# Optimization experiments

Measured on AMD Instinct MI355X. Metric: run time of the kernel, lower is better.

## Reference

```python
import jax, jax.numpy as jnp
import numpy as np

B, T, K = 128, 2048, 96  # batch, seq_len, num_tags


def setup_inputs() -> dict:
    key = jax.random.key(0)
    k1, k2, k3 = jax.random.split(key, 3)
    inputs = jax.random.normal(k1, (B, T, K), dtype=jnp.float32)
    tags = jax.random.randint(k2, (B, T), 0, K, dtype=jnp.int32)
    mask = jnp.ones((B, T), dtype=jnp.int32)
    transitions = jax.random.normal(k3, (K, K), dtype=jnp.float32) * 0.1
    return {"inputs": inputs, "tags": tags, "mask": mask, "transitions": transitions}


def _input_likelihood(inputs, mask, transitions):
    # Forward algorithm (log partition), no start/end transitions.
    logits_t = jnp.swapaxes(inputs, 0, 1)                     # [T,B,K]
    mask_t = jnp.swapaxes(mask, 0, 1)                         # [T,B]
    alpha0 = logits_t[0]                                      # [B,K]

    def step(alpha, xm):
        emit, m = xm                                          # emit [B,K], m [B]
        # inner[b,i,j] = alpha[b,i] + transitions[i,j] + emit[b,j]
        inner = alpha[:, :, None] + transitions[None, :, :] + emit[:, None, :]
        new = jax.nn.logsumexp(inner, axis=1)                 # [B,K]
        alpha = jnp.where(m[:, None] > 0, new, alpha)
        return alpha, None

    alpha, _ = jax.lax.scan(step, alpha0, (logits_t[1:], mask_t[1:]))
    return jax.nn.logsumexp(alpha, axis=-1)                   # [B]


def _joint_likelihood(inputs, tags, mask, transitions):
    # Score of the gold tag path.
    maskf = mask.astype(inputs.dtype)                         # [B,T]
    # transitions between consecutive tags, gated by mask[t+1]
    trans_sc = transitions[tags[:, :-1], tags[:, 1:]] * maskf[:, 1:]      # [B,T-1]
    # emissions for timesteps 0..T-2, gated by mask[t]
    emit_sc = jnp.take_along_axis(inputs[:, :-1, :], tags[:, :-1, None], axis=-1)[..., 0] * maskf[:, :-1]
    score = trans_sc.sum(-1) + emit_sc.sum(-1)                # [B]
    # last valid tag's emission, taken from the final timestep's logits (AllenNLP semantics)
    last_idx = jnp.sum(mask, axis=1) - 1                      # [B]
    last_tags = jnp.take_along_axis(tags, last_idx[:, None], axis=1)[:, 0]
    last_input_score = jnp.take_along_axis(inputs[:, -1, :], last_tags[:, None], axis=1)[:, 0]
    return score + last_input_score * maskf[:, -1]


def reference(inputs, tags, mask, transitions):
    log_denominator = _input_likelihood(inputs, mask, transitions)
    log_numerator = _joint_likelihood(inputs, tags, mask, transitions)
    return jnp.sum(log_numerator - log_denominator)  # reduction='sum'
```

## Files before the change

### kernel.cpp

```cpp
#include <hip/hip_runtime.h>


constexpr int K      = 96;
constexpr int NB     = 16;
constexpr int CHUNKS = 128;
constexpr int CLEN   = 16;
constexpr int WARM   = 8;
constexpr int B      = 128;

typedef __attribute__((ext_vector_type(8))) short bf16x8;
typedef __attribute__((ext_vector_type(4))) float f32x4;

__device__ __forceinline__ unsigned short f2bf(float f) {
  unsigned int b = __float_as_uint(f);
  return (unsigned short)((b + 0x7fff + ((b >> 16) & 1)) >> 16);
}
__device__ __forceinline__ float bf2f(unsigned short h) {
  return __uint_as_float(((unsigned int)h) << 16);
}
__device__ __forceinline__ unsigned int cvt_pk_bf16(float lo, float hi) {
  unsigned int r;
  asm volatile("v_cvt_pk_bf16_f32 %0, %1, %2" : "=v"(r) : "v"(lo), "v"(hi));
  return r;
}
__device__ __forceinline__ float lane_bcast(int addr4, float v) {
  return __int_as_float(__builtin_amdgcn_ds_bpermute(addr4, __float_as_int(v)));
}
__device__ __forceinline__ void dma16(const void* g, void* l) {
  __builtin_amdgcn_global_load_lds(
      (const __attribute__((address_space(1))) void*)g,
      (__attribute__((address_space(3))) void*)l, 16, 0, 0);
}

__global__ __launch_bounds__(64, 1) void crf_fwd_chunk(
    const float* __restrict__ inp,
    const int*   __restrict__ tags,
    const int*   __restrict__ mask,
    const float* __restrict__ trans,
    float* __restrict__ pden,
    float* __restrict__ pnum,
    float* __restrict__ pcnt,
    int T)
{
  const int l  = threadIdx.x;
  const int bl = l & 15;
  const int hi = l >> 4;
  const int g  = blockIdx.x;
  const int c  = blockIdx.y;
  const int b  = g * NB + bl;
  const int bcast = bl * 4;

  const int s_init = max(0, c * CLEN - WARM);
  const int s_A    = c * CLEN;
  const int s_end  = min(c * CLEN + CLEN, T - 1);

  __shared__ unsigned short Xs[NB][104];
  __shared__ float4 Ering[4][NB * K / 4];
  __shared__ float4 Edummy[64];

  bf16x8 A[6][3];
  #pragma unroll
  for (int jt = 0; jt < 6; ++jt) {
    #pragma unroll
    for (int kf = 0; kf < 3; ++kf) {
      const int j = jt * 16 + bl;
      #pragma unroll
      for (int e = 0; e < 8; ++e) {
        const int i = kf * 32 + hi * 8 + e;
        A[jt][kf][e] = (short)f2bf(__expf(trans[i * K + j]));
      }
    }
  }

  const float* ib  = inp  + (size_t)b * T * K;
  const int*   mb  = mask + (size_t)b * T;
  const int*   tgb = tags + (size_t)b * T;

  {
    const float* i0 = ib + (size_t)s_init * K;
    float4 e0[6];
    #pragma unroll
    for (int jt = 0; jt < 6; ++jt) {
      float4 v = *(const float4*)(i0 + jt * 16 + hi * 4);
      v.x = __expf(v.x); v.y = __expf(v.y); v.z = __expf(v.z); v.w = __expf(v.w);
      e0[jt] = v;
    }
    const float r0  = lane_bcast(bcast, e0[0].x);
    const float inv = 1.0f / r0;
    #pragma unroll
    for (int jt = 0; jt < 6; ++jt) {
      uint2 p;
      p.x = cvt_pk_bf16(e0[jt].x * inv, e0[jt].y * inv);
      p.y = cvt_pk_bf16(e0[jt].z * inv, e0[jt].w * inv);
      *(uint2*)&Xs[bl][jt * 16 + hi * 4] = p;
    }
  }
  double Mref = (double)ib[(size_t)s_init * K];

  bf16x8 Bf[3];
  #pragma unroll
  for (int kf = 0; kf < 3; ++kf)
    Bf[kf] = *(const bf16x8*)&Xs[bl][kf * 32 + hi * 8];

  unsigned mbits = 0;
  const int nsteps = s_end - s_init;
  #pragma unroll
  for (int k2 = 0; k2 < CLEN + WARM; ++k2)
    if (k2 < nsteps)
      mbits |= (mb[s_init + 1 + k2] != 0 ? 1u : 0u) << k2;

  const char* sp[6];
  #pragma unroll
  for (int p = 0; p < 6; ++p) {
    const int u  = p * 64 + l;
    const int r  = u / 24;
    const int x  = (u - r * 24) * 16;
    const int xs = x ^ ((r & 7) << 4);
    sp[p] = (const char*)(inp + ((size_t)(g * 16 + r) * T + (s_init + 1)) * K) + xs;
  }
  const int swr = (bl & 7) << 4;

  asm volatile("s_waitcnt vmcnt(0)" ::: "memory");
  __builtin_amdgcn_sched_barrier(0);

  auto issue_dma = [&](int s) {
    char* ld = (char*)&Ering[s & 3][0];
    const int off = (s - s_init - 1) * (K * 4);
    #pragma unroll
    for (int p = 0; p < 6; ++p)
      dma16(sp[p] + off, ld + p * 1024);
  };
  auto issue_dummy = [&]() {
    #pragma unroll
    for (int p = 0; p < 6; ++p)
      dma16(sp[p], (char*)&Edummy[0]);
  };
  auto issue = [&](int s) { if (s <= s_end) issue_dma(s); else issue_dummy(); };

  issue(s_init + 1); issue(s_init + 2); issue(s_init + 3); issue(s_init + 4);

  auto dostep = [&](int s, bool renorm) {
    asm volatile("s_waitcnt vmcnt(18)" ::: "memory");
    __builtin_amdgcn_sched_barrier(0);

    const char* slab = (const char*)&Ering[s & 3][0];
    float4 xe[6];
    #pragma unroll
    for (int jt = 0; jt < 6; ++jt) {
      const float4 e4 =
          *(const float4*)(slab + bl * 384 + ((jt * 64 + hi * 16) ^ swr));
      xe[jt].x = __expf(e4.x); xe[jt].y = __expf(e4.y);
      xe[jt].z = __expf(e4.z); xe[jt].w = __expf(e4.w);
    }
    __builtin_amdgcn_sched_barrier(0);
    issue(s + 4);
    __builtin_amdgcn_sched_barrier(0);

    f32x4 acc[6];
    #pragma unroll
    for (int jt = 0; jt < 6; ++jt) {
      f32x4 a = {0.f, 0.f, 0.f, 0.f};
      a = __builtin_amdgcn_mfma_f32_16x16x32_bf16(A[jt][0], Bf[0], a, 0, 0, 0);
      a = __builtin_amdgcn_mfma_f32_16x16x32_bf16(A[jt][1], Bf[1], a, 0, 0, 0);
      a = __builtin_amdgcn_mfma_f32_16x16x32_bf16(A[jt][2], Bf[2], a, 0, 0, 0);
      acc[jt] = a;
    }
    const bool mm = ((mbits >> (s - s_init - 1)) & 1u) != 0u;
    float inv = 1.0f;
    if (renorm) {
      const float r = lane_bcast(bcast, acc[0][0]);
      inv = 1.0f / r;
      if (mm) Mref += (double)__logf(r);
    }
    if (mm) {
      #pragma unroll
      for (int jt = 0; jt < 6; ++jt) {
        uint2 p;
        p.x = cvt_pk_bf16(acc[jt][0] * inv * xe[jt].x,
                          acc[jt][1] * inv * xe[jt].y);
        p.y = cvt_pk_bf16(acc[jt][2] * inv * xe[jt].z,
                          acc[jt][3] * inv * xe[jt].w);
        *(uint2*)&Xs[bl][jt * 16 + hi * 4] = p;
      }
    }
    #pragma unroll
    for (int kf = 0; kf < 3; ++kf)
      Bf[kf] = *(const bf16x8*)&Xs[bl][kf * 32 + hi * 8];
  };

  auto phi = [&]() -> double {
    float sum = 0.f;
    #pragma unroll
    for (int u = 0; u < 24; ++u) sum += bf2f(Xs[bl][hi * 24 + u]);
    sum += __shfl_xor(sum, 16);
    sum += __shfl_xor(sum, 32);
    return Mref + (double)__logf(sum);
  };

  double phiA = 0.0;
  int s = s_init + 1;
  while (s + 1 <= s_end) {
    dostep(s, false);
    dostep(s + 1, true);
    if (s + 1 == s_A) phiA = phi();
    s += 2;
  }
  if (s <= s_end) { dostep(s, true); ++s; }
  const double phiB = phi();

  if (hi == 0) pden[c * B + b] = (float)(phiB - phiA);

  const int t0 = c * CLEN;
  float nacc = 0.f, mcnt = 0.f;
  #pragma unroll
  for (int k = 0; k < CLEN / 4; ++k) {
    const int t  = t0 + 4 * k + hi;
    const int mt = mb[t];
    mcnt += (float)mt;
    if (t < T - 1) {
      const int tg  = tgb[t];
      const int tg1 = tgb[t + 1];
      nacc = fmaf(trans[tg * K + tg1], (float)mb[t + 1], nacc);
      nacc = fmaf(ib[(size_t)t * K + tg], (float)mt, nacc);
    }
  }
  nacc += __shfl_xor(nacc, 16); nacc += __shfl_xor(nacc, 32);
  mcnt += __shfl_xor(mcnt, 16); mcnt += __shfl_xor(mcnt, 32);
  if (hi == 0) {
    pnum[c * B + b] = nacc;
    pcnt[c * B + b] = mcnt;
  }
}

__global__ __launch_bounds__(128) void crf_reduce(
    const float* __restrict__ inp, const int* __restrict__ tags,
    const int* __restrict__ mask,
    const float* __restrict__ pden, const float* __restrict__ pnum,
    const float* __restrict__ pcnt, float* __restrict__ out, int T)
{
  const int b = threadIdx.x;
  float den = 0.f, num = 0.f, cnt = 0.f;
  for (int c = 0; c < CHUNKS; ++c) {
    den += pden[c * B + b];
    num += pnum[c * B + b];
    cnt += pcnt[c * B + b];
  }
  const int last_idx = (int)cnt - 1;
  float last_sc = 0.f;
  if (last_idx >= 0) {
    const int lt = tags[(size_t)b * T + last_idx];
    last_sc = inp[((size_t)b * T + (T - 1)) * K + lt]
            * (float)mask[(size_t)b * T + T - 1];
  }
  __shared__ float red[128];
  red[b] = num + last_sc - den;
  __syncthreads();
  #pragma unroll
  for (int s = 64; s > 0; s >>= 1) {
    if (b < s) red[b] += red[b + s];
    __syncthreads();
  }
  if (b == 0) out[0] = red[0];
}

extern "C" void kernel_launch(void* const* d_in, const int* in_sizes, int n_in,
                              void* d_out, int out_size, void* d_ws, size_t ws_size,
                              hipStream_t stream)
{
  const float* inp   = (const float*)d_in[0];
  const int*   tags  = (const int*)  d_in[1];
  const int*   mask  = (const int*)  d_in[2];
  const float* trans = (const float*)d_in[3];
  float*       out   = (float*)d_out;

  const int BT = in_sizes[1];
  const int T  = BT / B;

  float* pden = (float*)d_ws;
  float* pnum = pden + CHUNKS * B;
  float* pcnt = pnum + CHUNKS * B;

  dim3 grid(B / NB, CHUNKS);
  crf_fwd_chunk<<<grid, 64, 0, stream>>>(inp, tags, mask, trans,
                                         pden, pnum, pcnt, T);
  crf_reduce<<<1, 128, 0, stream>>>(inp, tags, mask, pden, pnum, pcnt, out, T);

  (void)n_in; (void)out_size; (void)ws_size;
}
```

Measured before the change: 46.84 us.

## Batch emission prefetch into four-step double-buffered super-steps with contiguous row loads

The per-timestep LDS DMA ring (four slots of one step each, one wait per step) becomes a double-buffered super-step scheme. Each super-step loads four consecutive timesteps per batch row, so every row becomes a contiguous 1536-byte span. Loads are issued two super-steps ahead and waited on once per four steps, which is meant to improve coalescing and cut per-step wait and issue overhead. In exchange it uses more LDS, and clamped out-of-range loads near the tail are issued for nothing.

```diff
diff --git a/kernel.cpp b/kernel.cpp
--- a/kernel.cpp
+++ b/kernel.cpp
@@ -7,6 +7,7 @@
 constexpr int CLEN   = 16;
 constexpr int WARM   = 8;
 constexpr int B      = 128;
+constexpr int SS     = 4;
 
 typedef __attribute__((ext_vector_type(8))) short bf16x8;
 typedef __attribute__((ext_vector_type(4))) float f32x4;
@@ -55,8 +56,7 @@
   const int s_end  = min(c * CLEN + CLEN, T - 1);
 
   __shared__ unsigned short Xs[NB][104];
-  __shared__ float4 Ering[4][NB * K / 4];
-  __shared__ float4 Edummy[64];
+  __shared__ char Ering[2][NB * SS * K * 4];
 
   bf16x8 A[6][3];
   #pragma unroll
@@ -109,53 +109,50 @@
     if (k2 < nsteps)
       mbits |= (mb[s_init + 1 + k2] != 0 ? 1u : 0u) << k2;
 
-  const char* sp[6];
-  #pragma unroll
-  for (int p = 0; p < 6; ++p) {
-    const int u  = p * 64 + l;
-    const int r  = u / 24;
-    const int x  = (u - r * 24) * 16;
-    const int xs = x ^ ((r & 7) << 4);
-    sp[p] = (const char*)(inp + ((size_t)(g * 16 + r) * T + (s_init + 1)) * K) + xs;
-  }
+  int drp[3], xp[3];
+  const char* rb[3];
+  #pragma unroll
+  for (int p = 0; p < 3; ++p) {
+    const int q = p * 1024 + l * 16;
+    drp[p] = q / 1536;
+    xp[p]  = q - drp[p] * 1536;
+    rb[p]  = (const char*)(inp + (size_t)(g * 16 + drp[p]) * T * K);
+  }
+  const size_t rowpair = (size_t)2 * T * K * 4;
+  const char* lim = (const char*)inp + (size_t)B * T * K * 4 - 16;
   const int swr = (bl & 7) << 4;
 
   asm volatile("s_waitcnt vmcnt(0)" ::: "memory");
   __builtin_amdgcn_sched_barrier(0);
 
-  auto issue_dma = [&](int s) {
-    char* ld = (char*)&Ering[s & 3][0];
-    const int off = (s - s_init - 1) * (K * 4);
-    #pragma unroll
-    for (int p = 0; p < 6; ++p)
-      dma16(sp[p] + off, ld + p * 1024);
+  auto issue_super = [&](int kk) {
+    const int s0 = s_init + 1 + SS * kk;
+    char* dst = &Ering[kk & 1][0];
+    #pragma unroll
+    for (int m = 0; m < 8; ++m) {
+      #pragma unroll
+      for (int p = 0; p < 3; ++p) {
+        const int sw = ((2 * m + drp[p]) & 7) << 4;
+        const char* src = rb[p] + (size_t)m * rowpair
+                        + (size_t)s0 * (K * 4) + (xp[p] ^ sw);
+        if (src > lim) src = lim;
+        dma16(src, dst + (m * 3 + p) * 1024);
+      }
+    }
   };
-  auto issue_dummy = [&]() {
-    #pragma unroll
-    for (int p = 0; p < 6; ++p)
-      dma16(sp[p], (char*)&Edummy[0]);
-  };
-  auto issue = [&](int s) { if (s <= s_end) issue_dma(s); else issue_dummy(); };
-
-  issue(s_init + 1); issue(s_init + 2); issue(s_init + 3); issue(s_init + 4);
-
-  auto dostep = [&](int s, bool renorm) {
-    asm volatile("s_waitcnt vmcnt(18)" ::: "memory");
-    __builtin_amdgcn_sched_barrier(0);
-
-    const char* slab = (const char*)&Ering[s & 3][0];
+
+  issue_super(0);
+  issue_super(1);
+
+  auto dostep = [&](int s, const char* slab, int u) {
     float4 xe[6];
     #pragma unroll
     for (int jt = 0; jt < 6; ++jt) {
-      const float4 e4 =
-          *(const float4*)(slab + bl * 384 + ((jt * 64 + hi * 16) ^ swr));
+      const float4 e4 = *(const float4*)(
+          slab + bl * 1536 + u * 384 + ((jt * 64 + hi * 16) ^ swr));
       xe[jt].x = __expf(e4.x); xe[jt].y = __expf(e4.y);
       xe[jt].z = __expf(e4.z); xe[jt].w = __expf(e4.w);
     }
-    __builtin_amdgcn_sched_barrier(0);
-    issue(s + 4);
-    __builtin_amdgcn_sched_barrier(0);
-
     f32x4 acc[6];
     #pragma unroll
     for (int jt = 0; jt < 6; ++jt) {
@@ -166,6 +163,7 @@
       acc[jt] = a;
     }
     const bool mm = ((mbits >> (s - s_init - 1)) & 1u) != 0u;
+    const bool renorm = (((s - s_init) & 1) == 0);
     float inv = 1.0f;
     if (renorm) {
       const float r = lane_bcast(bcast, acc[0][0]);
@@ -198,14 +196,24 @@
   };
 
   double phiA = 0.0;
-  int s = s_init + 1;
-  while (s + 1 <= s_end) {
-    dostep(s, false);
-    dostep(s + 1, true);
-    if (s + 1 == s_A) phiA = phi();
-    s += 2;
-  }
-  if (s <= s_end) { dostep(s, true); ++s; }
+  const int nss = (nsteps + SS - 1) / SS;
+  for (int k = 0; k < nss; ++k) {
+    asm volatile("s_waitcnt vmcnt(24)" ::: "memory");
+    __builtin_amdgcn_sched_barrier(0);
+    const char* slab = &Ering[k & 1][0];
+    const int s0 = s_init + 1 + SS * k;
+    #pragma unroll
+    for (int u = 0; u < SS; ++u) {
+      const int s = s0 + u;
+      if (s <= s_end) {
+        dostep(s, slab, u);
+        if (s == s_A) phiA = phi();
+      }
+    }
+    __builtin_amdgcn_sched_barrier(0);
+    issue_super(k + 2);
+    __builtin_amdgcn_sched_barrier(0);
+  }
   const double phiB = phi();
 
   if (hi == 0) pden[c * B + b] = (float)(phiB - phiA);
```

New measurement: 79.97 us. 1.71x slower.
